# Kernel tuning notes

Hardware: AMD Instinct MI355X
Metric: run time of the kernel (lower is better)

## Reference

```python
import jax, jax.numpy as jnp
import numpy as np

N = 50000
E = 800000
IN_C, HID_C, OUT_C = 256, 128, 64


def setup_inputs() -> dict:
    key = jax.random.key(0)
    k1, k2, k3, k4 = jax.random.split(key, 4)
    x = jax.random.normal(k1, (N, IN_C), dtype=jnp.float32)
    edge_index = jax.random.randint(k2, (2, E), 0, N, dtype=jnp.int64)
    # Glorot-ish init for GCN weights, zero bias (PyG default)
    W1 = jax.random.normal(k3, (IN_C, HID_C), dtype=jnp.float32) / np.sqrt(IN_C)
    b1 = jnp.zeros((HID_C,), dtype=jnp.float32)
    W2 = jax.random.normal(k4, (HID_C, OUT_C), dtype=jnp.float32) / np.sqrt(HID_C)
    b2 = jnp.zeros((OUT_C,), dtype=jnp.float32)
    return {"x": x, "edge_index": edge_index, "W1": W1, "b1": b1, "W2": W2, "b2": b2}


def _gcn_norm(edge_index, num_nodes):
    # Add self-loops, compute symmetric normalization D^-1/2 A D^-1/2 (PyG GCNConv default)
    loops = jnp.arange(num_nodes, dtype=edge_index.dtype)
    src = jnp.concatenate([edge_index[0], loops])  # message sources
    dst = jnp.concatenate([edge_index[1], loops])  # aggregation targets
    deg = jax.ops.segment_sum(jnp.ones_like(dst, dtype=jnp.float32), dst,
                              num_segments=num_nodes)
    dinv = jnp.where(deg > 0, jax.lax.rsqrt(deg), 0.0)
    norm = dinv[src] * dinv[dst]  # [E+N]
    return src, dst, norm


def _gcn_conv(x, W, b, src, dst, norm, num_nodes):
    h = x @ W                                   # [N, out]
    msg = h[src] * norm[:, None]                # gather + scale, [E+N, out]
    out = jax.ops.segment_sum(msg, dst, num_segments=num_nodes)  # scatter-add
    return out + b


def reference(x, edge_index, W1, b1, W2, b2):
    num_nodes = x.shape[0]
    src, dst, norm = _gcn_norm(edge_index, num_nodes)
    h = _gcn_conv(x, W1, b1, src, dst, norm, num_nodes)
    h = jax.nn.relu(h)
    # F.dropout(training=False) -> identity at inference
    return _gcn_conv(h, W2, b2, src, dst, norm, num_nodes)
```

## Files before the change

kernel.cpp:

```cpp
#include <hip/hip_runtime.h>
#include <hip/hip_bf16.h>


typedef __attribute__((ext_vector_type(8))) short short8;
typedef __attribute__((ext_vector_type(4))) float f32x4;

union BF8 {
    short8 s;
    uint4 u;
    __hip_bfloat162 h[4];
};

__device__ __forceinline__ unsigned short f32_to_bf16_rne(float f) {
    unsigned u = __float_as_uint(f);
    return (unsigned short)((u + 0x7fffu + ((u >> 16) & 1u)) >> 16);
}
__device__ __forceinline__ float bf_lo(unsigned v) { return __uint_as_float(v << 16); }
__device__ __forceinline__ float bf_hi(unsigned v) { return __uint_as_float(v & 0xffff0000u); }

#define ACHUNK 2048
#define BSH 6
#define BN 64
#define CAP 2048
#define EPT (CAP / 256)

__global__ void wfrag_zero_kernel(const float* __restrict__ W1, const float* __restrict__ W2,
                                  unsigned short* __restrict__ w1f,
                                  unsigned short* __restrict__ w2f,
                                  int* __restrict__ counts, int* __restrict__ bcursor,
                                  int n, int nbk) {
    int i = blockIdx.x * blockDim.x + threadIdx.x;
    if (i < n) counts[i] = 0;
    if (i < nbk) bcursor[i] = 0;
    const float* W;
    unsigned short* WF;
    int KS, NCOL, idx;
    if (i < 32768) {
        W = W1; WF = w1f; KS = 8; NCOL = 128; idx = i;
    } else if (i < 32768 + 8192) {
        W = W2; WF = w2f; KS = 4; NCOL = 64; idx = i - 32768;
    } else return;
    int j = idx & 7;
    int lane = (idx >> 3) & 63;
    int f = idx >> 9;
    int ks = f % KS, nt = f / KS;
    int m16 = lane & 15, quad = lane >> 4;
    int ncol = nt * 16 + m16;
    int k = ks * 32 + quad * 8 + j;
    WF[idx] = f32_to_bf16_rne(W[k * NCOL + ncol]);
}

__global__ __launch_bounds__(256) void gemm1_bucket_kernel(
    const float* __restrict__ A, const unsigned short* __restrict__ BFRAG,
    unsigned short* __restrict__ C, int M, int gGemm,
    const int* __restrict__ src, const int* __restrict__ dst,
    int* __restrict__ counts, int* __restrict__ bcursor,
    int2* __restrict__ tmp, int e, int nbk) {
    constexpr int NT = 8, KS = 8;
    constexpr int K = KS * 32;
    constexpr int LSTRIDE = K + 8;
    __shared__ char smem[64 * LSTRIDE * 2];

    const int tid = threadIdx.x;
    if ((int)blockIdx.x < gGemm) {
        unsigned short* Alds = (unsigned short*)smem;
        const int wave = tid >> 6, lane = tid & 63;
        const int quad = lane >> 4, m16 = lane & 15;
        const int rowBase = blockIdx.x * 64;

        constexpr int HALVES = K / 128;
#pragma unroll
        for (int h = 0; h < HALVES; h++) {
            f32x4 v[8];
#pragma unroll
            for (int it = 0; it < 8; it++) {
                int p = (h * 8 + it) * 1024 + tid * 4;
                int rg = rowBase + p / K;
                if (rg >= M) rg = M - 1;
                v[it] = *(const f32x4*)(A + (size_t)rg * K + (p % K));
            }
#pragma unroll
            for (int it = 0; it < 8; it++) {
                int p = (h * 8 + it) * 1024 + tid * 4;
                BF8 cv;
                cv.h[0] = __float22bfloat162_rn(make_float2(v[it].x, v[it].y));
                cv.h[1] = __float22bfloat162_rn(make_float2(v[it].z, v[it].w));
                *(uint2*)&Alds[(p / K) * LSTRIDE + (p % K)] = make_uint2(cv.u.x, cv.u.y);
            }
        }
        __syncthreads();

        const unsigned short* Afrag0 = &Alds[(wave * 16 + m16) * LSTRIDE + quad * 8];
        const uint4* Bfrag = (const uint4*)BFRAG + lane;

        f32x4 acc[NT];
#pragma unroll
        for (int nt = 0; nt < NT; nt++) acc[nt] = f32x4{0.f, 0.f, 0.f, 0.f};
#pragma unroll
        for (int ks = 0; ks < KS; ks++) {
            BF8 af;
            af.u = *(const uint4*)(Afrag0 + ks * 32);
#pragma unroll
            for (int nt = 0; nt < NT; nt++) {
                BF8 bf;
                bf.u = Bfrag[(nt * KS + ks) * 64];
                acc[nt] = __builtin_amdgcn_mfma_f32_16x16x32_bf16(af.s, bf.s, acc[nt], 0, 0, 0);
            }
        }
        const int rowOut = rowBase + wave * 16 + quad * 4;
#pragma unroll
        for (int nt = 0; nt < NT; nt++) {
#pragma unroll
            for (int r = 0; r < 4; r++) {
                int row = rowOut + r;
                if (row < M)
                    C[(size_t)row * 128 + nt * 16 + m16] = f32_to_bf16_rne(acc[nt][r]);
            }
        }
    } else {
        int* sdst = (int*)smem;
        int* hist = (int*)(smem + ACHUNK * 4);
        const int b0 = blockIdx.x - gGemm;
        const int start = b0 * ACHUNK;
        const int cnt = min(ACHUNK, e - start);
        for (int t = tid; t < nbk; t += 256) hist[t] = 0;
        __syncthreads();
        for (int i = tid; i < cnt; i += 256) {
            int d = dst[start + i];
            sdst[i] = d;
            atomicAdd(&counts[d], 1);
            atomicAdd(&hist[d >> BSH], 1);
        }
        __syncthreads();
        for (int t = tid; t < nbk; t += 256) {
            int h = hist[t];
            hist[t] = (h > 0) ? atomicAdd(&bcursor[t], h) : 0;
        }
        __syncthreads();
        for (int i = tid; i < cnt; i += 256) {
            int d = sdst[i];
            int slot = atomicAdd(&hist[d >> BSH], 1);
            if (slot < CAP)
                tmp[(size_t)(d >> BSH) * CAP + slot] = make_int2(src[start + i], d);
        }
    }
}

__global__ __launch_bounds__(256) void aggsort_gemm2_kernel(
    const int* __restrict__ counts, const int2* __restrict__ tmp,
    const int* __restrict__ bcursor,
    const unsigned short* __restrict__ hb,
    const float* __restrict__ bias1,
    const unsigned short* __restrict__ w2frag,
    int2* __restrict__ sedge, int2* __restrict__ nodeRange,
    unsigned short* __restrict__ h2, int n) {
    constexpr int LSTRIDE = 136;
    __shared__ int ecnt[BN];
    __shared__ int estart[BN];
    __shared__ int lcur[BN];
    __shared__ float ndinv[BN];
    __shared__ int ssrc[CAP];
    __shared__ float swt[CAP];
    __shared__ unsigned short a1lds[BN * LSTRIDE];

    const int tid = threadIdx.x;
    const int b = blockIdx.x;
    const int nodeBase = b << BSH;
    const int nNodes = min(BN, n - nodeBase);
    const int cnt = min(bcursor[b], CAP);

    if (tid < BN) ecnt[tid] = 0;
    __syncthreads();

    int2 er[EPT];
#pragma unroll
    for (int j = 0; j < EPT; j++) {
        int i = tid + j * 256;
        if (i < cnt) {
            int2 r = tmp[(size_t)b * CAP + i];
            er[j] = r;
            atomicAdd(&ecnt[r.y - nodeBase], 1);
        } else {
            er[j].x = -1;
            er[j].y = 0;
        }
    }
    __syncthreads();

    if (tid < BN) {
        int c = ecnt[tid];
        int x = c;
#pragma unroll
        for (int off = 1; off < 64; off <<= 1) {
            int y = __shfl_up(x, off, 64);
            if (tid >= off) x += y;
        }
        int st = x - c;
        estart[tid] = st;
        lcur[tid] = st;
        ndinv[tid] = (tid < nNodes) ? rsqrtf((float)counts[nodeBase + tid] + 1.0f) : 0.0f;
        if (tid < nNodes) nodeRange[nodeBase + tid] = make_int2(b * CAP + st, c);
    }
    __syncthreads();

#pragma unroll
    for (int j = 0; j < EPT; j++) {
        if (er[j].x >= 0) {
            int ln = er[j].y - nodeBase;
            float w = rsqrtf((float)counts[er[j].x] + 1.0f) * ndinv[ln];
            int pos = atomicAdd(&lcur[ln], 1);
            ssrc[pos] = er[j].x;
            swt[pos] = w;
            sedge[(size_t)b * CAP + pos] = make_int2(er[j].x, __float_as_int(w));
        }
    }
    __syncthreads();

    const int sub = tid & 15;
    const int qw = tid >> 4;
    for (int pass = 0; pass < BN / 16; pass++) {
        int ln = pass * 16 + qw;
        float a0 = 0.f, a1 = 0.f, a2 = 0.f, a3 = 0.f;
        float a4 = 0.f, a5 = 0.f, a6 = 0.f, a7 = 0.f;
        if (ln < nNodes) {
            int node = nodeBase + ln;
            float di = ndinv[ln];
            float d2 = di * di;
            uint4 sv = ((const uint4*)(hb + (size_t)node * 128))[sub];
            a0 = d2 * bf_lo(sv.x); a1 = d2 * bf_hi(sv.x);
            a2 = d2 * bf_lo(sv.y); a3 = d2 * bf_hi(sv.y);
            a4 = d2 * bf_lo(sv.z); a5 = d2 * bf_hi(sv.z);
            a6 = d2 * bf_lo(sv.w); a7 = d2 * bf_hi(sv.w);
            int beg = estart[ln];
            int end = beg + ecnt[ln];
            int i = beg;
            for (; i + 4 <= end; i += 4) {
                int s[4]; float w[4]; uint4 v[4];
#pragma unroll
                for (int j = 0; j < 4; j++) { s[j] = ssrc[i + j]; w[j] = swt[i + j]; }
#pragma unroll
                for (int j = 0; j < 4; j++)
                    v[j] = ((const uint4*)(hb + (size_t)s[j] * 128))[sub];
#pragma unroll
                for (int j = 0; j < 4; j++) {
                    a0 = fmaf(w[j], bf_lo(v[j].x), a0); a1 = fmaf(w[j], bf_hi(v[j].x), a1);
                    a2 = fmaf(w[j], bf_lo(v[j].y), a2); a3 = fmaf(w[j], bf_hi(v[j].y), a3);
                    a4 = fmaf(w[j], bf_lo(v[j].z), a4); a5 = fmaf(w[j], bf_hi(v[j].z), a5);
                    a6 = fmaf(w[j], bf_lo(v[j].w), a6); a7 = fmaf(w[j], bf_hi(v[j].w), a7);
                }
            }
            for (; i < end; ++i) {
                int s = ssrc[i];
                float w = swt[i];
                uint4 v = ((const uint4*)(hb + (size_t)s * 128))[sub];
                a0 = fmaf(w, bf_lo(v.x), a0); a1 = fmaf(w, bf_hi(v.x), a1);
                a2 = fmaf(w, bf_lo(v.y), a2); a3 = fmaf(w, bf_hi(v.y), a3);
                a4 = fmaf(w, bf_lo(v.z), a4); a5 = fmaf(w, bf_hi(v.z), a5);
                a6 = fmaf(w, bf_lo(v.w), a6); a7 = fmaf(w, bf_hi(v.w), a7);
            }
            float4 b0v = ((const float4*)bias1)[sub * 2];
            float4 b1v = ((const float4*)bias1)[sub * 2 + 1];
            a0 = fmaxf(a0 + b0v.x, 0.f); a1 = fmaxf(a1 + b0v.y, 0.f);
            a2 = fmaxf(a2 + b0v.z, 0.f); a3 = fmaxf(a3 + b0v.w, 0.f);
            a4 = fmaxf(a4 + b1v.x, 0.f); a5 = fmaxf(a5 + b1v.y, 0.f);
            a6 = fmaxf(a6 + b1v.z, 0.f); a7 = fmaxf(a7 + b1v.w, 0.f);
        }
        BF8 p;
        p.h[0] = __float22bfloat162_rn(make_float2(a0, a1));
        p.h[1] = __float22bfloat162_rn(make_float2(a2, a3));
        p.h[2] = __float22bfloat162_rn(make_float2(a4, a5));
        p.h[3] = __float22bfloat162_rn(make_float2(a6, a7));
        *(uint4*)&a1lds[ln * LSTRIDE + sub * 8] = p.u;
    }
    __syncthreads();

    const int wave = tid >> 6, lane = tid & 63;
    const int quad = lane >> 4, m16 = lane & 15;
    const unsigned short* Afrag0 = &a1lds[(wave * 16 + m16) * LSTRIDE + quad * 8];
    const uint4* Bfrag = (const uint4*)w2frag + lane;

    f32x4 acc[4];
#pragma unroll
    for (int nt = 0; nt < 4; nt++) acc[nt] = f32x4{0.f, 0.f, 0.f, 0.f};
#pragma unroll
    for (int ks = 0; ks < 4; ks++) {
        BF8 af;
        af.u = *(const uint4*)(Afrag0 + ks * 32);
#pragma unroll
        for (int nt = 0; nt < 4; nt++) {
            BF8 bf;
            bf.u = Bfrag[(nt * 4 + ks) * 64];
            acc[nt] = __builtin_amdgcn_mfma_f32_16x16x32_bf16(af.s, bf.s, acc[nt], 0, 0, 0);
        }
    }
    const int rowOut = wave * 16 + quad * 4;
#pragma unroll
    for (int nt = 0; nt < 4; nt++) {
#pragma unroll
        for (int r = 0; r < 4; r++) {
            int row = rowOut + r;
            if (row < nNodes)
                h2[(size_t)(nodeBase + row) * 64 + nt * 16 + m16] =
                    f32_to_bf16_rne(acc[nt][r]);
        }
    }
}

__global__ __launch_bounds__(256) void agg64_kernel(
    const int2* __restrict__ nodeRange, const int2* __restrict__ sedge,
    const unsigned short* __restrict__ hb, const int* __restrict__ counts,
    const float* __restrict__ bias, float* __restrict__ out, int n) {
    int node = blockIdx.x * 16 + (threadIdx.x >> 4);
    if (node >= n) return;
    int sub = threadIdx.x & 15;
    float di = rsqrtf((float)counts[node] + 1.0f);
    float d2 = di * di;
    uint2 sv = ((const uint2*)(hb + (size_t)node * 64))[sub];
    float a0 = d2 * bf_lo(sv.x), a1 = d2 * bf_hi(sv.x);
    float a2 = d2 * bf_lo(sv.y), a3 = d2 * bf_hi(sv.y);
    int2 nr = nodeRange[node];
    int beg = nr.x, end = nr.x + nr.y;
    int i = beg;
    for (; i + 8 <= end; i += 8) {
        int2 e[8];
        uint2 v[8];
#pragma unroll
        for (int j = 0; j < 8; j++) e[j] = sedge[i + j];
#pragma unroll
        for (int j = 0; j < 8; j++)
            v[j] = ((const uint2*)(hb + (size_t)e[j].x * 64))[sub];
#pragma unroll
        for (int j = 0; j < 8; j++) {
            float w = __int_as_float(e[j].y);
            a0 = fmaf(w, bf_lo(v[j].x), a0); a1 = fmaf(w, bf_hi(v[j].x), a1);
            a2 = fmaf(w, bf_lo(v[j].y), a2); a3 = fmaf(w, bf_hi(v[j].y), a3);
        }
    }
    for (; i + 4 <= end; i += 4) {
        int2 e[4];
        uint2 v[4];
#pragma unroll
        for (int j = 0; j < 4; j++) e[j] = sedge[i + j];
#pragma unroll
        for (int j = 0; j < 4; j++)
            v[j] = ((const uint2*)(hb + (size_t)e[j].x * 64))[sub];
#pragma unroll
        for (int j = 0; j < 4; j++) {
            float w = __int_as_float(e[j].y);
            a0 = fmaf(w, bf_lo(v[j].x), a0); a1 = fmaf(w, bf_hi(v[j].x), a1);
            a2 = fmaf(w, bf_lo(v[j].y), a2); a3 = fmaf(w, bf_hi(v[j].y), a3);
        }
    }
    for (; i < end; ++i) {
        int2 e = sedge[i];
        float w = __int_as_float(e.y);
        uint2 v = ((const uint2*)(hb + (size_t)e.x * 64))[sub];
        a0 = fmaf(w, bf_lo(v.x), a0); a1 = fmaf(w, bf_hi(v.x), a1);
        a2 = fmaf(w, bf_lo(v.y), a2); a3 = fmaf(w, bf_hi(v.y), a3);
    }
    float4 bv = ((const float4*)bias)[sub];
    ((float4*)(out + (size_t)node * 64))[sub] =
        make_float4(a0 + bv.x, a1 + bv.y, a2 + bv.z, a3 + bv.w);
}

extern "C" void kernel_launch(void* const* d_in, const int* in_sizes, int n_in,
                              void* d_out, int out_size, void* d_ws, size_t ws_size,
                              hipStream_t stream) {
    const float* x  = (const float*)d_in[0];
    const int*   ei = (const int*)d_in[1];
    const float* W1 = (const float*)d_in[2];
    const float* b1 = (const float*)d_in[3];
    const float* W2 = (const float*)d_in[4];
    const float* b2 = (const float*)d_in[5];
    float* out = (float*)d_out;

    const int IN_C = 256;
    const int N = in_sizes[0] / IN_C;
    const int E = in_sizes[1] / 2;
    const int* srcA = ei;
    const int* dstA = ei + E;

    char* ws = (char*)d_ws;
    const size_t KB = 1024, MB = 1024 * 1024;
    int*            counts    = (int*)(ws);
    int*            bcursor   = (int*)(ws + 256 * KB);
    unsigned short* w1f       = (unsigned short*)(ws + 1 * MB);
    unsigned short* w2f       = (unsigned short*)(ws + 1 * MB + 64 * KB);
    int2*           tmp       = (int2*)(ws + 2 * MB);
    int2*           sedge     = (int2*)(ws + 16 * MB);
    int2*           nodeRange = (int2*)(ws + 30 * MB);
    unsigned short* h1b       = (unsigned short*)(ws + 31 * MB);
    unsigned short* h2b       = (unsigned short*)(ws + 44 * MB);

    const int NB = (N + BN - 1) / BN;
    const int gGemm = (N + 63) / 64;
    const int nbA = (E + ACHUNK - 1) / ACHUNK;
    const int gWfrag = (max(N, 32768 + 8192) + 255) / 256;

    wfrag_zero_kernel<<<gWfrag, 256, 0, stream>>>(W1, W2, w1f, w2f, counts, bcursor, N, NB);
    gemm1_bucket_kernel<<<gGemm + nbA, 256, 0, stream>>>(
        x, w1f, h1b, N, gGemm, srcA, dstA, counts, bcursor, tmp, E, NB);
    aggsort_gemm2_kernel<<<NB, 256, 0, stream>>>(
        counts, tmp, bcursor, h1b, b1, w2f, sedge, nodeRange, h2b, N);
    agg64_kernel<<<(N + 15) / 16, 256, 0, stream>>>(nodeRange, sedge, h2b, counts, b2, out, N);
}
```

Measured before the change: 202.1 us.

## Stage GEMM outputs through LDS for coalesced stores and unroll gathers by eight

Both MFMA epilogues now write bf16 results into LDS first and then store full rows with 16-byte vector writes. Previously each thread issued scattered 2-byte global stores. The layer-1 aggregation gather loop gets an 8-way unrolled path so more loads are in flight. Degrees are taken from the locally known edge count instead of a reload from the counts array, and agg64 gets a launch-bounds occupancy hint. The costs are extra LDS traffic, two more barriers per block, and higher register pressure from the wider unroll.

After: 204.5 us. About the same (+1.2%).

```diff
diff --git a/kernel.cpp b/kernel.cpp
--- a/kernel.cpp
+++ b/kernel.cpp
@@ -107,19 +107,27 @@
                 acc[nt] = __builtin_amdgcn_mfma_f32_16x16x32_bf16(af.s, bf.s, acc[nt], 0, 0, 0);
             }
         }
-        const int rowOut = rowBase + wave * 16 + quad * 4;
-#pragma unroll
-        for (int nt = 0; nt < NT; nt++) {
-#pragma unroll
-            for (int r = 0; r < 4; r++) {
-                int row = rowOut + r;
-                if (row < M)
-                    C[(size_t)row * 128 + nt * 16 + m16] = f32_to_bf16_rne(acc[nt][r]);
-            }
+        __syncthreads();
+        unsigned short* Clds = (unsigned short*)smem;
+        const int rowL = wave * 16 + quad * 4;
+#pragma unroll
+        for (int nt = 0; nt < NT; nt++)
+#pragma unroll
+            for (int r = 0; r < 4; r++)
+                Clds[(rowL + r) * 136 + nt * 16 + m16] = f32_to_bf16_rne(acc[nt][r]);
+        __syncthreads();
+#pragma unroll
+        for (int ps = 0; ps < 4; ps++) {
+            int idx = ps * 256 + tid;
+            int r = idx >> 4;
+            int c = (idx & 15) * 8;
+            int row = rowBase + r;
+            if (row < M)
+                *(uint4*)&C[(size_t)row * 128 + c] = *(const uint4*)&Clds[r * 136 + c];
         }
     } else {
         int* sdst = (int*)smem;
-        int* hist = (int*)(smem + ACHUNK * 4);
+        int* hist = (int*)((char*)smem + ACHUNK * 4);
         const int b0 = blockIdx.x - gGemm;
         const int start = b0 * ACHUNK;
         const int cnt = min(ACHUNK, e - start);
@@ -198,7 +206,7 @@
         int st = x - c;
         estart[tid] = st;
         lcur[tid] = st;
-        ndinv[tid] = (tid < nNodes) ? rsqrtf((float)counts[nodeBase + tid] + 1.0f) : 0.0f;
+        ndinv[tid] = rsqrtf((float)c + 1.0f);
         if (tid < nNodes) nodeRange[nodeBase + tid] = make_int2(b * CAP + st, c);
     }
     __syncthreads();
@@ -234,6 +242,21 @@
             int beg = estart[ln];
             int end = beg + ecnt[ln];
             int i = beg;
+            for (; i + 8 <= end; i += 8) {
+                int s[8]; float w[8]; uint4 v[8];
+#pragma unroll
+                for (int j = 0; j < 8; j++) { s[j] = ssrc[i + j]; w[j] = swt[i + j]; }
+#pragma unroll
+                for (int j = 0; j < 8; j++)
+                    v[j] = ((const uint4*)(hb + (size_t)s[j] * 128))[sub];
+#pragma unroll
+                for (int j = 0; j < 8; j++) {
+                    a0 = fmaf(w[j], bf_lo(v[j].x), a0); a1 = fmaf(w[j], bf_hi(v[j].x), a1);
+                    a2 = fmaf(w[j], bf_lo(v[j].y), a2); a3 = fmaf(w[j], bf_hi(v[j].y), a3);
+                    a4 = fmaf(w[j], bf_lo(v[j].z), a4); a5 = fmaf(w[j], bf_hi(v[j].z), a5);
+                    a6 = fmaf(w[j], bf_lo(v[j].w), a6); a7 = fmaf(w[j], bf_hi(v[j].w), a7);
+                }
+            }
             for (; i + 4 <= end; i += 4) {
                 int s[4]; float w[4]; uint4 v[4];
 #pragma unroll
@@ -293,32 +316,37 @@
             acc[nt] = __builtin_amdgcn_mfma_f32_16x16x32_bf16(af.s, bf.s, acc[nt], 0, 0, 0);
         }
     }
-    const int rowOut = wave * 16 + quad * 4;
-#pragma unroll
-    for (int nt = 0; nt < 4; nt++) {
-#pragma unroll
-        for (int r = 0; r < 4; r++) {
-            int row = rowOut + r;
-            if (row < nNodes)
-                h2[(size_t)(nodeBase + row) * 64 + nt * 16 + m16] =
-                    f32_to_bf16_rne(acc[nt][r]);
-        }
-    }
-}
-
-__global__ __launch_bounds__(256) void agg64_kernel(
+    __syncthreads();
+    const int rowL = wave * 16 + quad * 4;
+#pragma unroll
+    for (int nt = 0; nt < 4; nt++)
+#pragma unroll
+        for (int r = 0; r < 4; r++)
+            a1lds[(rowL + r) * 72 + nt * 16 + m16] = f32_to_bf16_rne(acc[nt][r]);
+    __syncthreads();
+#pragma unroll
+    for (int ps = 0; ps < 2; ps++) {
+        int idx = ps * 256 + tid;
+        int r = idx >> 3;
+        int c = (idx & 7) * 8;
+        if (r < nNodes)
+            *(uint4*)&h2[(size_t)(nodeBase + r) * 64 + c] = *(const uint4*)&a1lds[r * 72 + c];
+    }
+}
+
+__global__ __launch_bounds__(256, 8) void agg64_kernel(
     const int2* __restrict__ nodeRange, const int2* __restrict__ sedge,
-    const unsigned short* __restrict__ hb, const int* __restrict__ counts,
+    const unsigned short* __restrict__ hb,
     const float* __restrict__ bias, float* __restrict__ out, int n) {
     int node = blockIdx.x * 16 + (threadIdx.x >> 4);
     if (node >= n) return;
     int sub = threadIdx.x & 15;
-    float di = rsqrtf((float)counts[node] + 1.0f);
+    int2 nr = nodeRange[node];
+    float di = rsqrtf((float)nr.y + 1.0f);
     float d2 = di * di;
     uint2 sv = ((const uint2*)(hb + (size_t)node * 64))[sub];
     float a0 = d2 * bf_lo(sv.x), a1 = d2 * bf_hi(sv.x);
     float a2 = d2 * bf_lo(sv.y), a3 = d2 * bf_hi(sv.y);
-    int2 nr = nodeRange[node];
     int beg = nr.x, end = nr.x + nr.y;
     int i = beg;
     for (; i + 8 <= end; i += 8) {
@@ -402,5 +430,5 @@
         x, w1f, h1b, N, gGemm, srcA, dstA, counts, bcursor, tmp, E, NB);
     aggsort_gemm2_kernel<<<NB, 256, 0, stream>>>(
         counts, tmp, bcursor, h1b, b1, w2f, sedge, nodeRange, h2b, N);
-    agg64_kernel<<<(N + 15) / 16, 256, 0, stream>>>(nodeRange, sedge, h2b, counts, b2, out, N);
-}
+    agg64_kernel<<<(N + 15) / 16, 256, 0, stream>>>(nodeRange, sedge, h2b, b2, out, N);
+}
```
